# Performance work log

Measured on AMD Instinct MI355X. Metric: run time of the kernel, lower is better.

## Reference

```python
import jax, jax.numpy as jnp
import numpy as np

N = 100000   # nodes
E1 = 1600000 # message-passing edges (graph)
E2 = 1600000 # scoring edges (edge_graph)
IN, H1, H2, MH, MO = 128, 128, 64, 128, 1


def setup_inputs() -> dict:
    key = jax.random.key(0)
    ks = jax.random.split(key, 16)
    s = 0.05
    return {
        "inputs": jax.random.normal(ks[0], (N, IN), jnp.float32),
        "edge_src": jax.random.randint(ks[1], (E1,), 0, N, jnp.int32),
        "edge_dst": jax.random.randint(ks[2], (E1,), 0, N, jnp.int32),
        "score_src": jax.random.randint(ks[3], (E2,), 0, N, jnp.int32),
        "score_dst": jax.random.randint(ks[4], (E2,), 0, N, jnp.int32),
        # SAGEConv layer 1: out = x @ W_self + mean_neigh(x) @ W_neigh + b
        "W_self1": jax.random.normal(ks[5], (IN, H1), jnp.float32) * s,
        "W_neigh1": jax.random.normal(ks[6], (IN, H1), jnp.float32) * s,
        "b1": jnp.zeros((H1,), jnp.float32),
        # SAGEConv layer 2
        "W_self2": jax.random.normal(ks[7], (H1, H2), jnp.float32) * s,
        "W_neigh2": jax.random.normal(ks[8], (H1, H2), jnp.float32) * s,
        "b2": jnp.zeros((H2,), jnp.float32),
        # edge MLP
        "W_mlp1": jax.random.normal(ks[9], (2 * H2, MH), jnp.float32) * s,
        "b_mlp1": jnp.zeros((MH,), jnp.float32),
        "W_mlp2": jax.random.normal(ks[10], (MH, MO), jnp.float32) * s,
        "b_mlp2": jnp.zeros((MO,), jnp.float32),
    }


def _sage_mean(h, edge_src, edge_dst, inv_deg, W_self, W_neigh, b):
    # mean aggregation of in-neighbor (src) features at dst nodes
    agg = jax.ops.segment_sum(h[edge_src], edge_dst, num_segments=N) * inv_deg
    return h @ W_self + agg @ W_neigh + b


def reference(inputs, edge_src, edge_dst, score_src, score_dst,
              W_self1, W_neigh1, b1, W_self2, W_neigh2, b2,
              W_mlp1, b_mlp1, W_mlp2, b_mlp2):
    # in-degree of each dst node (zero-degree -> mean of 0, matches DGL)
    deg = jax.ops.segment_sum(jnp.ones((E1,), jnp.float32), edge_dst, num_segments=N)
    inv_deg = (1.0 / jnp.maximum(deg, 1.0))[:, None]

    h = jax.nn.relu(_sage_mean(inputs, edge_src, edge_dst, inv_deg, W_self1, W_neigh1, b1))
    # dropout is identity at inference
    h = jax.nn.relu(_sage_mean(h, edge_src, edge_dst, inv_deg, W_self2, W_neigh2, b2))

    # apply_edges: gather src/dst, concat, MLP + sigmoid
    h_concat = jnp.concatenate([h[score_src], h[score_dst]], axis=1)  # [E2, 2*H2]
    h2 = jax.nn.relu(h_concat @ W_mlp1 + b_mlp1)
    score = jax.nn.sigmoid(h2 @ W_mlp2 + b_mlp2)  # [E2, 1]
    return score, h
```

## Files before the change

kernel.cpp:

```cpp
#include <hip/hip_runtime.h>

#define NN  100000
#define EE1 1600000
#define EE2 1600000

#define NPB 256
#define NB  ((NN + NPB - 1) / NPB)
#define EPB 4096
#define NABLK ((EE1 + EPB - 1) / EPB)

typedef unsigned short u16;
typedef unsigned int   u32;
typedef short s16x8 __attribute__((ext_vector_type(8)));
typedef float f32x4 __attribute__((ext_vector_type(4)));

__device__ __forceinline__ float bf2f(u32 u) {
    union { u32 i; float f; } v; v.i = (u & 0xffffu) << 16; return v.f;
}
__device__ __forceinline__ u16 f2bf(float f) {
    u32 x = __builtin_bit_cast(u32, f);
    return (u16)((x + 0x7fffu + ((x >> 16) & 1u)) >> 16);
}
__device__ __forceinline__ u32 pack2(float a, float b) {
    return (u32)f2bf(a) | ((u32)f2bf(b) << 16);
}
__device__ __forceinline__ int clampi(int v, int hi) {
    return v < 0 ? 0 : (v > hi ? hi : v);
}

__global__ void k_cast(const float* __restrict__ X, u16* __restrict__ Xb) {
    int i = blockIdx.x * 256 + threadIdx.x;
    if (i < NN * 128 / 4) {
        float4 v = *(const float4*)&X[i * 4];
        union { u16 h[4]; uint2 u; } o;
        o.h[0] = f2bf(v.x); o.h[1] = f2bf(v.y);
        o.h[2] = f2bf(v.z); o.h[3] = f2bf(v.w);
        *(uint2*)&Xb[i * 4] = o.u;
    }
}


__global__ __launch_bounds__(256) void k_binA0(const int* __restrict__ ed,
                                               int* __restrict__ bucketCnt) {
    __shared__ int hist[NB];
    const int t = threadIdx.x;
    for (int i = t; i < NB; i += 256) hist[i] = 0;
    __syncthreads();
    const int e0 = blockIdx.x * EPB;
    const int e1 = min(e0 + EPB, EE1);
    for (int e = e0 + t; e < e1; e += 256)
        atomicAdd(&hist[clampi(ed[e], NN - 1) >> 8], 1);
    __syncthreads();
    for (int i = t; i < NB; i += 256)
        if (hist[i]) atomicAdd(&bucketCnt[i], hist[i]);
}

__global__ void k_scanB(const int* __restrict__ cnt, int* __restrict__ bbase,
                        int* __restrict__ bcur) {
    __shared__ int l[512];
    const int t = threadIdx.x;
    const int v = (t < NB) ? cnt[t] : 0;
    l[t] = v;
    __syncthreads();
    for (int d = 1; d < 512; d <<= 1) {
        int x = (t >= d) ? l[t - d] : 0;
        __syncthreads();
        l[t] += x;
        __syncthreads();
    }
    if (t < NB) { const int excl = l[t] - v; bbase[t] = excl; bcur[t] = excl; }
    if (t == 0) bbase[NB] = EE1;
}

__global__ __launch_bounds__(256) void k_binA(const int* __restrict__ es,
                                              const int* __restrict__ ed,
                                              int* __restrict__ bucketCur,
                                              u32* __restrict__ buck) {
    __shared__ int hist[NB];
    __shared__ int base[NB];
    const int t = threadIdx.x;
    for (int i = t; i < NB; i += 256) hist[i] = 0;
    __syncthreads();
    const int e0 = blockIdx.x * EPB;
    const int e1 = min(e0 + EPB, EE1);
    for (int e = e0 + t; e < e1; e += 256)
        atomicAdd(&hist[clampi(ed[e], NN - 1) >> 8], 1);
    __syncthreads();
    for (int i = t; i < NB; i += 256) {
        const int h = hist[i];
        base[i] = h ? atomicAdd(&bucketCur[i], h) : 0;
        hist[i] = 0;
    }
    __syncthreads();
    for (int e = e0 + t; e < e1; e += 256) {
        const int d = clampi(ed[e], NN - 1);
        const int s = clampi(es[e], NN - 1);
        const int b = d >> 8;
        const int p = base[b] + atomicAdd(&hist[b], 1);
        buck[p] = ((u32)(d & 255) << 24) | (u32)s;
    }
}

__global__ __launch_bounds__(256) void k_binB(const u32* __restrict__ buck,
                                              const int* __restrict__ bbase,
                                              int* __restrict__ offs,
                                              int* __restrict__ csr) {
    __shared__ int hist[NPB];
    __shared__ int scan[NPB];
    const int t = threadIdx.x;
    const int b = blockIdx.x;
    const int base = bbase[b], end = bbase[b + 1];
    hist[t] = 0;
    __syncthreads();
    for (int i = base + t; i < end; i += 256)
        atomicAdd(&hist[buck[i] >> 24], 1);
    __syncthreads();
    const int v = hist[t];
    scan[t] = v;
    __syncthreads();
    for (int d = 1; d < 256; d <<= 1) {
        int x = (t >= d) ? scan[t - d] : 0;
        __syncthreads();
        scan[t] += x;
        __syncthreads();
    }
    const int excl = scan[t] - v;
    const int node = b * NPB + t;
    if (node < NN) offs[node] = base + excl;
    if (node == NN - 1) offs[NN] = EE1;
    hist[t] = base + excl;
    __syncthreads();
    for (int i = base + t; i < end; i += 256) {
        const u32 pv = buck[i];
        const int p = atomicAdd(&hist[pv >> 24], 1);
        csr[p] = (int)(pv & 0xFFFFFFu);
    }
}

__global__ void k_prep(const float* __restrict__ Ws1, const float* __restrict__ Wn1,
                       const float* __restrict__ Ws2, const float* __restrict__ Wn2,
                       const float* __restrict__ Wm1,
                       u16* __restrict__ WT1, u16* __restrict__ WT2, u16* __restrict__ WTM) {
    int i = blockIdx.x * 256 + threadIdx.x;
    if (i < 32768) {
        int f = i, j = f & 7, L = (f >> 3) & 63, t2 = f >> 9;
        int s = t2 & 7, c = t2 >> 3;
        int k = s * 32 + ((L >> 4) << 3) + j, co = (c << 4) + (L & 15);
        WT1[f] = f2bf((k < 128) ? Ws1[k * 128 + co] : Wn1[(k - 128) * 128 + co]);
    } else if (i < 49152) {
        int f = i - 32768, j = f & 7, L = (f >> 3) & 63, t2 = f >> 9;
        int s = t2 & 7, c = t2 >> 3;
        int k = s * 32 + ((L >> 4) << 3) + j, co = (c << 4) + (L & 15);
        WT2[f] = f2bf((k < 128) ? Ws2[k * 64 + co] : Wn2[(k - 128) * 64 + co]);
    } else {
        int f = i - 49152, j = f & 7, L = (f >> 3) & 63, t2 = f >> 9;
        int s = t2 & 3, c = t2 >> 2;
        int k = s * 32 + ((L >> 4) << 3) + j, co = (c << 4) + (L & 15);
        WTM[f] = f2bf(Wm1[k * 128 + co]);
    }
}

__global__ void k_bias(const float* b1, const float* b2, const float* bm1, const float* w2, const float* b2m,
                       float* __restrict__ blob) {
    const int t = threadIdx.x;
    if (t < 128)      blob[t] = b1[t];
    else if (t < 192) blob[t] = b2[t - 128];
    else if (t < 320) blob[t] = bm1[t - 192];
    else if (t < 448) blob[t] = w2[t - 320];
    else if (t == 448) blob[t] = b2m[0];
}

__device__ __forceinline__ void acc8(float* a, uint4 r) {
    a[0] += bf2f(r.x); a[1] += bf2f(r.x >> 16);
    a[2] += bf2f(r.y); a[3] += bf2f(r.y >> 16);
    a[4] += bf2f(r.z); a[5] += bf2f(r.z >> 16);
    a[6] += bf2f(r.w); a[7] += bf2f(r.w >> 16);
}

template<int CO, bool DUALOUT>
__global__ __launch_bounds__(256) void k_layer(const u16* __restrict__ Xb,
                                               const u16* __restrict__ WT,
                                               const int* __restrict__ offs,
                                               const int* __restrict__ csr,
                                               const float* __restrict__ biasf,
                                               u16* __restrict__ Hb,
                                               float* __restrict__ Hf) {
    constexpr int K = 128, KV = 8, CT = CO / 16, RS = K + 8;
    __shared__ __align__(16) u16 aggT[64 * RS];
    const int t = threadIdx.x, lane = t & 63, w = t >> 6;
    const int g = lane >> 4, f = lane & 15;
    const int rbase = blockIdx.x * 64;

    for (int i = 0; i < 4; ++i) {
        const int lrow = w * 16 + i * 4 + g;
        const int node = rbase + lrow;
        float acc[8] = {0.f, 0.f, 0.f, 0.f, 0.f, 0.f, 0.f, 0.f};
        float sc = 0.f;
        if (node < NN) {
            int beg = offs[node], end = offs[node + 1];
            if (beg < 0) beg = 0;
            if (end > EE1) end = EE1;
            if (end < beg) end = beg;
            sc = 1.0f / (float)max(end - beg, 1);
            int e = beg;
            for (; e + 4 <= end; e += 4) {
                int n0 = clampi(csr[e],     NN - 1);
                int n1 = clampi(csr[e + 1], NN - 1);
                int n2 = clampi(csr[e + 2], NN - 1);
                int n3 = clampi(csr[e + 3], NN - 1);
                uint4 r0 = *(const uint4*)&Xb[(size_t)n0 * K + f * 8];
                uint4 r1 = *(const uint4*)&Xb[(size_t)n1 * K + f * 8];
                uint4 r2 = *(const uint4*)&Xb[(size_t)n2 * K + f * 8];
                uint4 r3 = *(const uint4*)&Xb[(size_t)n3 * K + f * 8];
                acc8(acc, r0); acc8(acc, r1); acc8(acc, r2); acc8(acc, r3);
            }
            for (; e < end; ++e) {
                int n = clampi(csr[e], NN - 1);
                uint4 r = *(const uint4*)&Xb[(size_t)n * K + f * 8];
                acc8(acc, r);
            }
        }
        uint4 o;
        o.x = pack2(acc[0] * sc, acc[1] * sc);
        o.y = pack2(acc[2] * sc, acc[3] * sc);
        o.z = pack2(acc[4] * sc, acc[5] * sc);
        o.w = pack2(acc[6] * sc, acc[7] * sc);
        *(uint4*)&aggT[lrow * RS + f * 8] = o;
    }
    __syncthreads();

    const int nidx = lane & 15, quad = lane >> 4;
    int arow = rbase + w * 16 + nidx;
    if (arow > NN - 1) arow = NN - 1;
    const u16* xu = &Xb[(size_t)arow * K];
    const u16* grow = &aggT[(w * 16 + nidx) * RS];
    f32x4 acc[CT] = {};
#pragma unroll
    for (int s = 0; s < KV; ++s) {
        s16x8 a = (s < 4) ? *(const s16x8*)&xu[s * 32 + quad * 8]
                          : *(const s16x8*)&grow[(s - 4) * 32 + quad * 8];
#pragma unroll
        for (int c = 0; c < CT; ++c) {
            s16x8 b = *(const s16x8*)&WT[((c * KV + s) * 64 + lane) * 8];
            acc[c] = __builtin_amdgcn_mfma_f32_16x16x32_bf16(a, b, acc[c], 0, 0, 0);
        }
    }
#pragma unroll
    for (int c = 0; c < CT; ++c) {
        int col = c * 16 + nidx;
        float bv = biasf[col];
#pragma unroll
        for (int r = 0; r < 4; ++r) {
            int orow = rbase + w * 16 + quad * 4 + r;
            if (orow < NN) {
                float hv = fmaxf(acc[c][r] + bv, 0.f);
                Hb[(size_t)orow * CO + col] = f2bf(hv);
                if (DUALOUT) Hf[(size_t)orow * CO + col] = hv;
            }
        }
    }
}

__global__ __launch_bounds__(256) void k_edge(const u16* __restrict__ H2,
                                              const u16* __restrict__ WTM,
                                              const int* __restrict__ es, const int* __restrict__ ed,
                                              const float* __restrict__ blob,
                                              float* __restrict__ out) {
    const int t = threadIdx.x, lane = t & 63, w = t >> 6;
    const int nidx = lane & 15, quad = lane >> 4;
    const int base = blockIdx.x * 256 + w * 64;

    const u16* rs[4];
    const u16* rd[4];
#pragma unroll
    for (int tt = 0; tt < 4; ++tt) {
        const int e = base + tt * 16 + nidx;
        const int ns = clampi(es[e], NN - 1);
        const int nd = clampi(ed[e], NN - 1);
        rs[tt] = H2 + (size_t)ns * 64;
        rd[tt] = H2 + (size_t)nd * 64;
    }
    s16x8 a[4][4];
#pragma unroll
    for (int tt = 0; tt < 4; ++tt) {
        a[tt][0] = *(const s16x8*)&rs[tt][     quad * 8];
        a[tt][1] = *(const s16x8*)&rs[tt][32 + quad * 8];
        a[tt][2] = *(const s16x8*)&rd[tt][     quad * 8];
        a[tt][3] = *(const s16x8*)&rd[tt][32 + quad * 8];
    }

    float sum[4][4] = {};
#pragma unroll
    for (int c = 0; c < 8; ++c) {
        const s16x8 b0 = *(const s16x8*)&WTM[((c * 4 + 0) * 64 + lane) * 8];
        const s16x8 b1 = *(const s16x8*)&WTM[((c * 4 + 1) * 64 + lane) * 8];
        const s16x8 b2 = *(const s16x8*)&WTM[((c * 4 + 2) * 64 + lane) * 8];
        const s16x8 b3 = *(const s16x8*)&WTM[((c * 4 + 3) * 64 + lane) * 8];
        const int col = c * 16 + nidx;
        const float bb = blob[192 + col], ww = blob[320 + col];
#pragma unroll
        for (int tt = 0; tt < 4; ++tt) {
            f32x4 acc = {};
            acc = __builtin_amdgcn_mfma_f32_16x16x32_bf16(a[tt][0], b0, acc, 0, 0, 0);
            acc = __builtin_amdgcn_mfma_f32_16x16x32_bf16(a[tt][1], b1, acc, 0, 0, 0);
            acc = __builtin_amdgcn_mfma_f32_16x16x32_bf16(a[tt][2], b2, acc, 0, 0, 0);
            acc = __builtin_amdgcn_mfma_f32_16x16x32_bf16(a[tt][3], b3, acc, 0, 0, 0);
#pragma unroll
            for (int r = 0; r < 4; ++r)
                sum[tt][r] += fmaxf(acc[r] + bb, 0.f) * ww;
        }
    }

#pragma unroll
    for (int tt = 0; tt < 4; ++tt) {
#pragma unroll
        for (int r = 0; r < 4; ++r) {
            sum[tt][r] += __shfl_xor(sum[tt][r], 1, 64);
            sum[tt][r] += __shfl_xor(sum[tt][r], 2, 64);
            sum[tt][r] += __shfl_xor(sum[tt][r], 4, 64);
            sum[tt][r] += __shfl_xor(sum[tt][r], 8, 64);
        }
    }
    if (nidx == 0) {
        const float bb2 = blob[448];
#pragma unroll
        for (int tt = 0; tt < 4; ++tt) {
            f32x4 o;
#pragma unroll
            for (int r = 0; r < 4; ++r) {
                float x = sum[tt][r] + bb2;
                o[r] = 1.f / (1.f + __expf(-x));
            }
            *(f32x4*)&out[base + tt * 16 + quad * 4] = o;
        }
    }
}

extern "C" void kernel_launch(void* const* d_in, const int* in_sizes, int n_in,
                              void* d_out, int out_size, void* d_ws, size_t ws_size,
                              hipStream_t stream) {
    const float* X      = (const float*)d_in[0];
    const int*   esrc   = (const int*)d_in[1];
    const int*   edst   = (const int*)d_in[2];
    const int*   ssrc   = (const int*)d_in[3];
    const int*   sdst   = (const int*)d_in[4];
    const float* Wself1 = (const float*)d_in[5];
    const float* Wneigh1= (const float*)d_in[6];
    const float* b1     = (const float*)d_in[7];
    const float* Wself2 = (const float*)d_in[8];
    const float* Wneigh2= (const float*)d_in[9];
    const float* b2     = (const float*)d_in[10];
    const float* Wmlp1  = (const float*)d_in[11];
    const float* bmlp1  = (const float*)d_in[12];
    const float* Wmlp2  = (const float*)d_in[13];
    const float* bmlp2  = (const float*)d_in[14];

    char* ws = (char*)d_ws;
    int*   offs = (int*)(ws + 0);
    int*   csr  = (int*)(ws + 400128);
    u16*   WTM  = (u16*)(ws + 6800128);
    u16*   WT1  = (u16*)(ws + 6832896);
    u16*   WT2  = (u16*)(ws + 6898432);
    float* blob = (float*)(ws + 6931200);
    u16*   H1   = (u16*)(ws + 6933504);
    u16*   H2b  = (u16*)(ws + 32533504);
    u32*   buck = (u32*)(ws + 6933504);
    int*   bcnt = (int*)(ws + 13333504);
    int*   bbase= (int*)(ws + 13335168);
    int*   bcur = (int*)(ws + 13336832);

    float* outScore = (float*)d_out;
    float* Hf       = (float*)d_out + EE2;
    u16*   Xb       = (u16*)((char*)d_out + 6400000);

    k_cast<<<(NN * 128 / 4 + 255) / 256, 256, 0, stream>>>(X, Xb);
    hipMemsetAsync(bcnt, 0, NB * sizeof(int), stream);
    k_binA0<<<NABLK, 256, 0, stream>>>(edst, bcnt);
    k_scanB<<<1, 512, 0, stream>>>(bcnt, bbase, bcur);
    k_binA <<<NABLK, 256, 0, stream>>>(esrc, edst, bcur, buck);
    k_binB <<<NB, 256, 0, stream>>>(buck, bbase, offs, csr);
    k_prep<<<256, 256, 0, stream>>>(Wself1, Wneigh1, Wself2, Wneigh2, Wmlp1, WT1, WT2, WTM);
    k_bias<<<1, 512, 0, stream>>>(b1, b2, bmlp1, Wmlp2, bmlp2, blob);

    const int nblk = (NN + 63) / 64;
    k_layer<128, false><<<nblk, 256, 0, stream>>>(Xb, WT1, offs, csr, blob,       H1,  nullptr);
    k_layer<64,  true> <<<nblk, 256, 0, stream>>>(H1, WT2, offs, csr, blob + 128, H2b, Hf);
    k_edge<<<EE2 / 256, 256, 0, stream>>>(H2b, WTM, ssrc, sdst, blob, outScore);
}
```

Before: 468.0 us.

## Balance neighbor aggregation by splitting block edge range evenly across thread groups

The CSR entries now keep the local destination row in the top byte. Each 64-node block's contiguous edge range is split evenly across 16 groups of 16 threads, instead of assigning whole nodes per group. Each group accumulates runs that share a row and flushes them with shared-memory float atomics into an fp32 aggregation tile. The mean scaling and bf16 conversion move into the MFMA operand load. This targets load imbalance from varying node degrees, at the cost of shared atomics, a larger fp32 LDS tile (lower occupancy) and extra conversion work.

New measurement: 532.3 us. 1.14x slower.

```diff
diff --git a/kernel.cpp b/kernel.cpp
--- a/kernel.cpp
+++ b/kernel.cpp
@@ -104,7 +104,7 @@
 __global__ __launch_bounds__(256) void k_binB(const u32* __restrict__ buck,
                                               const int* __restrict__ bbase,
                                               int* __restrict__ offs,
-                                              int* __restrict__ csr) {
+                                              u32* __restrict__ csr) {
     __shared__ int hist[NPB];
     __shared__ int scan[NPB];
     const int t = threadIdx.x;
@@ -133,7 +133,7 @@
     for (int i = base + t; i < end; i += 256) {
         const u32 pv = buck[i];
         const int p = atomicAdd(&hist[pv >> 24], 1);
-        csr[p] = (int)(pv & 0xFFFFFFu);
+        csr[p] = pv;
     }
 }
 
@@ -181,51 +181,56 @@
 __global__ __launch_bounds__(256) void k_layer(const u16* __restrict__ Xb,
                                                const u16* __restrict__ WT,
                                                const int* __restrict__ offs,
-                                               const int* __restrict__ csr,
+                                               const u32* __restrict__ csr,
                                                const float* __restrict__ biasf,
                                                u16* __restrict__ Hb,
                                                float* __restrict__ Hf) {
-    constexpr int K = 128, KV = 8, CT = CO / 16, RS = K + 8;
-    __shared__ __align__(16) u16 aggT[64 * RS];
+    constexpr int K = 128, KV = 8, CT = CO / 16, FS = 132;
+    __shared__ __align__(16) float aggF[64 * FS];
     const int t = threadIdx.x, lane = t & 63, w = t >> 6;
-    const int g = lane >> 4, f = lane & 15;
     const int rbase = blockIdx.x * 64;
-
-    for (int i = 0; i < 4; ++i) {
-        const int lrow = w * 16 + i * 4 + g;
-        const int node = rbase + lrow;
-        float acc[8] = {0.f, 0.f, 0.f, 0.f, 0.f, 0.f, 0.f, 0.f};
-        float sc = 0.f;
-        if (node < NN) {
-            int beg = offs[node], end = offs[node + 1];
-            if (beg < 0) beg = 0;
-            if (end > EE1) end = EE1;
-            if (end < beg) end = beg;
-            sc = 1.0f / (float)max(end - beg, 1);
-            int e = beg;
-            for (; e + 4 <= end; e += 4) {
-                int n0 = clampi(csr[e],     NN - 1);
-                int n1 = clampi(csr[e + 1], NN - 1);
-                int n2 = clampi(csr[e + 2], NN - 1);
-                int n3 = clampi(csr[e + 3], NN - 1);
-                uint4 r0 = *(const uint4*)&Xb[(size_t)n0 * K + f * 8];
-                uint4 r1 = *(const uint4*)&Xb[(size_t)n1 * K + f * 8];
-                uint4 r2 = *(const uint4*)&Xb[(size_t)n2 * K + f * 8];
-                uint4 r3 = *(const uint4*)&Xb[(size_t)n3 * K + f * 8];
-                acc8(acc, r0); acc8(acc, r1); acc8(acc, r2); acc8(acc, r3);
+    const int grp = t >> 4, f = t & 15;
+
+    for (int i = t; i < 64 * FS; i += 256) aggF[i] = 0.f;
+    __syncthreads();
+
+    {
+        const int ebeg = offs[rbase];
+        const int eend = offs[min(rbase + 64, NN)];
+        const int elen = eend - ebeg;
+        const int myBeg = ebeg + ((elen * grp) >> 4);
+        const int myEnd = ebeg + ((elen * (grp + 1)) >> 4);
+        float acc[8] = {};
+        int curRow = -1;
+        for (int e = myBeg; e < myEnd; e += 4) {
+            const int n = min(myEnd - e, 4);
+            u32 pv[4]; uint4 r[4];
+#pragma unroll
+            for (int k = 0; k < 4; ++k) if (k < n) pv[k] = csr[e + k];
+#pragma unroll
+            for (int k = 0; k < 4; ++k) if (k < n)
+                r[k] = *(const uint4*)&Xb[(size_t)(pv[k] & 0xFFFFFFu) * K + f * 8];
+#pragma unroll
+            for (int k = 0; k < 4; ++k) if (k < n) {
+                const int lr = (int)(pv[k] >> 24) & 63;
+                if (lr != curRow) {
+                    if (curRow >= 0) {
+                        float* dst = &aggF[curRow * FS + f * 8];
+#pragma unroll
+                        for (int j = 0; j < 8; ++j) atomicAdd(&dst[j], acc[j]);
+                    }
+#pragma unroll
+                    for (int j = 0; j < 8; ++j) acc[j] = 0.f;
+                    curRow = lr;
+                }
+                acc8(acc, r[k]);
             }
-            for (; e < end; ++e) {
-                int n = clampi(csr[e], NN - 1);
-                uint4 r = *(const uint4*)&Xb[(size_t)n * K + f * 8];
-                acc8(acc, r);
-            }
-        }
-        uint4 o;
-        o.x = pack2(acc[0] * sc, acc[1] * sc);
-        o.y = pack2(acc[2] * sc, acc[3] * sc);
-        o.z = pack2(acc[4] * sc, acc[5] * sc);
-        o.w = pack2(acc[6] * sc, acc[7] * sc);
-        *(uint4*)&aggT[lrow * RS + f * 8] = o;
+        }
+        if (curRow >= 0) {
+            float* dst = &aggF[curRow * FS + f * 8];
+#pragma unroll
+            for (int j = 0; j < 8; ++j) atomicAdd(&dst[j], acc[j]);
+        }
     }
     __syncthreads();
 
@@ -233,16 +238,30 @@
     int arow = rbase + w * 16 + nidx;
     if (arow > NN - 1) arow = NN - 1;
     const u16* xu = &Xb[(size_t)arow * K];
-    const u16* grow = &aggT[(w * 16 + nidx) * RS];
-    f32x4 acc[CT] = {};
+    const float* gf = &aggF[(w * 16 + nidx) * FS];
+    const int dg = offs[min(arow + 1, NN)] - offs[arow];
+    const float sc = 1.0f / (float)max(dg, 1);
+    f32x4 accv[CT] = {};
 #pragma unroll
     for (int s = 0; s < KV; ++s) {
-        s16x8 a = (s < 4) ? *(const s16x8*)&xu[s * 32 + quad * 8]
-                          : *(const s16x8*)&grow[(s - 4) * 32 + quad * 8];
+        s16x8 a;
+        if (s < 4) {
+            a = *(const s16x8*)&xu[s * 32 + quad * 8];
+        } else {
+            const float* g8 = &gf[(s - 4) * 32 + quad * 8];
+            f32x4 v0 = *(const f32x4*)&g8[0];
+            f32x4 v1 = *(const f32x4*)&g8[4];
+            union { u32 u[4]; s16x8 h; } cv;
+            cv.u[0] = pack2(v0[0] * sc, v0[1] * sc);
+            cv.u[1] = pack2(v0[2] * sc, v0[3] * sc);
+            cv.u[2] = pack2(v1[0] * sc, v1[1] * sc);
+            cv.u[3] = pack2(v1[2] * sc, v1[3] * sc);
+            a = cv.h;
+        }
 #pragma unroll
         for (int c = 0; c < CT; ++c) {
             s16x8 b = *(const s16x8*)&WT[((c * KV + s) * 64 + lane) * 8];
-            acc[c] = __builtin_amdgcn_mfma_f32_16x16x32_bf16(a, b, acc[c], 0, 0, 0);
+            accv[c] = __builtin_amdgcn_mfma_f32_16x16x32_bf16(a, b, accv[c], 0, 0, 0);
         }
     }
 #pragma unroll
@@ -253,7 +272,7 @@
         for (int r = 0; r < 4; ++r) {
             int orow = rbase + w * 16 + quad * 4 + r;
             if (orow < NN) {
-                float hv = fmaxf(acc[c][r] + bv, 0.f);
+                float hv = fmaxf(accv[c][r] + bv, 0.f);
                 Hb[(size_t)orow * CO + col] = f2bf(hv);
                 if (DUALOUT) Hf[(size_t)orow * CO + col] = hv;
             }
@@ -357,7 +376,7 @@
 
     char* ws = (char*)d_ws;
     int*   offs = (int*)(ws + 0);
-    int*   csr  = (int*)(ws + 400128);
+    u32*   csr  = (u32*)(ws + 400128);
     u16*   WTM  = (u16*)(ws + 6800128);
     u16*   WT1  = (u16*)(ws + 6832896);
     u16*   WT2  = (u16*)(ws + 6898432);
```

## Double layer block size to 512 threads and split MFMA column tiles across waves

Applied to the files above, without the earlier changes.

The SAGE layer kernel now runs 8 waves per 64-node block instead of 4. Each 16-lane group aggregates 2 nodes instead of 4, and pairs of waves split the output column tiles of the MFMA GEMM. The CSR array now keeps the packed bucket word, and the layer masks the low 24 bits in place of a separate mask-and-clamp step. The aim is more memory-level parallelism for the gather-bound aggregation, at the cost of higher register pressure per block and duplicated A-fragment loads across paired waves.

Result: faster. 448.1 us (-4.3%).

```diff
diff --git a/kernel.cpp b/kernel.cpp
--- a/kernel.cpp
+++ b/kernel.cpp
@@ -104,7 +104,7 @@
 __global__ __launch_bounds__(256) void k_binB(const u32* __restrict__ buck,
                                               const int* __restrict__ bbase,
                                               int* __restrict__ offs,
-                                              int* __restrict__ csr) {
+                                              u32* __restrict__ csr) {
     __shared__ int hist[NPB];
     __shared__ int scan[NPB];
     const int t = threadIdx.x;
@@ -133,7 +133,7 @@
     for (int i = base + t; i < end; i += 256) {
         const u32 pv = buck[i];
         const int p = atomicAdd(&hist[pv >> 24], 1);
-        csr[p] = (int)(pv & 0xFFFFFFu);
+        csr[p] = pv;
     }
 }
 
@@ -178,21 +178,22 @@
 }
 
 template<int CO, bool DUALOUT>
-__global__ __launch_bounds__(256) void k_layer(const u16* __restrict__ Xb,
+__global__ __launch_bounds__(512) void k_layer(const u16* __restrict__ Xb,
                                                const u16* __restrict__ WT,
                                                const int* __restrict__ offs,
-                                               const int* __restrict__ csr,
+                                               const u32* __restrict__ csr,
                                                const float* __restrict__ biasf,
                                                u16* __restrict__ Hb,
                                                float* __restrict__ Hf) {
-    constexpr int K = 128, KV = 8, CT = CO / 16, RS = K + 8;
+    constexpr int K = 128, KV = 8, CT = CO / 16, CH = CT / 2, RS = K + 8;
     __shared__ __align__(16) u16 aggT[64 * RS];
     const int t = threadIdx.x, lane = t & 63, w = t >> 6;
     const int g = lane >> 4, f = lane & 15;
+    const int grp = w * 4 + g;
     const int rbase = blockIdx.x * 64;
 
-    for (int i = 0; i < 4; ++i) {
-        const int lrow = w * 16 + i * 4 + g;
+    for (int i = 0; i < 2; ++i) {
+        const int lrow = grp * 2 + i;
         const int node = rbase + lrow;
         float acc[8] = {0.f, 0.f, 0.f, 0.f, 0.f, 0.f, 0.f, 0.f};
         float sc = 0.f;
@@ -204,19 +205,16 @@
             sc = 1.0f / (float)max(end - beg, 1);
             int e = beg;
             for (; e + 4 <= end; e += 4) {
-                int n0 = clampi(csr[e],     NN - 1);
-                int n1 = clampi(csr[e + 1], NN - 1);
-                int n2 = clampi(csr[e + 2], NN - 1);
-                int n3 = clampi(csr[e + 3], NN - 1);
-                uint4 r0 = *(const uint4*)&Xb[(size_t)n0 * K + f * 8];
-                uint4 r1 = *(const uint4*)&Xb[(size_t)n1 * K + f * 8];
-                uint4 r2 = *(const uint4*)&Xb[(size_t)n2 * K + f * 8];
-                uint4 r3 = *(const uint4*)&Xb[(size_t)n3 * K + f * 8];
+                u32 p0 = csr[e], p1 = csr[e + 1], p2 = csr[e + 2], p3 = csr[e + 3];
+                uint4 r0 = *(const uint4*)&Xb[(size_t)(p0 & 0xFFFFFFu) * K + f * 8];
+                uint4 r1 = *(const uint4*)&Xb[(size_t)(p1 & 0xFFFFFFu) * K + f * 8];
+                uint4 r2 = *(const uint4*)&Xb[(size_t)(p2 & 0xFFFFFFu) * K + f * 8];
+                uint4 r3 = *(const uint4*)&Xb[(size_t)(p3 & 0xFFFFFFu) * K + f * 8];
                 acc8(acc, r0); acc8(acc, r1); acc8(acc, r2); acc8(acc, r3);
             }
             for (; e < end; ++e) {
-                int n = clampi(csr[e], NN - 1);
-                uint4 r = *(const uint4*)&Xb[(size_t)n * K + f * 8];
+                u32 p = csr[e];
+                uint4 r = *(const uint4*)&Xb[(size_t)(p & 0xFFFFFFu) * K + f * 8];
                 acc8(acc, r);
             }
         }
@@ -230,30 +228,32 @@
     __syncthreads();
 
     const int nidx = lane & 15, quad = lane >> 4;
-    int arow = rbase + w * 16 + nidx;
+    const int ws = w >> 1, ch = w & 1;
+    int arow = rbase + ws * 16 + nidx;
     if (arow > NN - 1) arow = NN - 1;
     const u16* xu = &Xb[(size_t)arow * K];
-    const u16* grow = &aggT[(w * 16 + nidx) * RS];
-    f32x4 acc[CT] = {};
+    const u16* grow = &aggT[(ws * 16 + nidx) * RS];
+    f32x4 accv[CH] = {};
 #pragma unroll
     for (int s = 0; s < KV; ++s) {
         s16x8 a = (s < 4) ? *(const s16x8*)&xu[s * 32 + quad * 8]
                           : *(const s16x8*)&grow[(s - 4) * 32 + quad * 8];
 #pragma unroll
-        for (int c = 0; c < CT; ++c) {
-            s16x8 b = *(const s16x8*)&WT[((c * KV + s) * 64 + lane) * 8];
-            acc[c] = __builtin_amdgcn_mfma_f32_16x16x32_bf16(a, b, acc[c], 0, 0, 0);
-        }
-    }
-#pragma unroll
-    for (int c = 0; c < CT; ++c) {
-        int col = c * 16 + nidx;
+        for (int c = 0; c < CH; ++c) {
+            const int cc = ch * CH + c;
+            s16x8 b = *(const s16x8*)&WT[((cc * KV + s) * 64 + lane) * 8];
+            accv[c] = __builtin_amdgcn_mfma_f32_16x16x32_bf16(a, b, accv[c], 0, 0, 0);
+        }
+    }
+#pragma unroll
+    for (int c = 0; c < CH; ++c) {
+        const int col = (ch * CH + c) * 16 + nidx;
         float bv = biasf[col];
 #pragma unroll
         for (int r = 0; r < 4; ++r) {
-            int orow = rbase + w * 16 + quad * 4 + r;
+            int orow = rbase + ws * 16 + quad * 4 + r;
             if (orow < NN) {
-                float hv = fmaxf(acc[c][r] + bv, 0.f);
+                float hv = fmaxf(accv[c][r] + bv, 0.f);
                 Hb[(size_t)orow * CO + col] = f2bf(hv);
                 if (DUALOUT) Hf[(size_t)orow * CO + col] = hv;
             }
@@ -357,7 +357,7 @@
 
     char* ws = (char*)d_ws;
     int*   offs = (int*)(ws + 0);
-    int*   csr  = (int*)(ws + 400128);
+    u32*   csr  = (u32*)(ws + 400128);
     u16*   WTM  = (u16*)(ws + 6800128);
     u16*   WT1  = (u16*)(ws + 6832896);
     u16*   WT2  = (u16*)(ws + 6898432);
@@ -383,7 +383,7 @@
     k_bias<<<1, 512, 0, stream>>>(b1, b2, bmlp1, Wmlp2, bmlp2, blob);
 
     const int nblk = (NN + 63) / 64;
-    k_layer<128, false><<<nblk, 256, 0, stream>>>(Xb, WT1, offs, csr, blob,       H1,  nullptr);
-    k_layer<64,  true> <<<nblk, 256, 0, stream>>>(H1, WT2, offs, csr, blob + 128, H2b, Hf);
+    k_layer<128, false><<<nblk, 512, 0, stream>>>(Xb, WT1, offs, csr, blob,       H1,  nullptr);
+    k_layer<64,  true> <<<nblk, 512, 0, stream>>>(H1, WT2, offs, csr, blob + 128, H2b, Hf);
     k_edge<<<EE2 / 256, 256, 0, stream>>>(H2b, WTM, ssrc, sdst, blob, outScore);
 }
```
